# Optimization experiments

Hardware: AMD Instinct MI355X
Metric: run time of the kernel (lower is better)

## Reference

```python
import jax, jax.numpy as jnp
import numpy as np
from jax import lax

B, T, V, E, H, O = 32, 64, 30000, 64, 64, 7


def setup_inputs() -> dict:
    key = jax.random.key(0)
    ks = jax.random.split(key, 17)
    s_in = 1.0 / np.sqrt(E)
    s_h = 1.0 / np.sqrt(H)
    inp = {
        "x": jax.random.uniform(ks[0], (B, T, V), dtype=jnp.float32),
        "vocab_embed": 0.02 * jax.random.normal(ks[1], (V, E), dtype=jnp.float32),
        "W_ir": s_in * jax.random.normal(ks[2], (H, E), dtype=jnp.float32),
        "W_iz": s_in * jax.random.normal(ks[3], (H, E), dtype=jnp.float32),
        "W_in": s_in * jax.random.normal(ks[4], (H, E), dtype=jnp.float32),
        "W_hr": s_h * jax.random.normal(ks[5], (H, H), dtype=jnp.float32),
        "W_hz": s_h * jax.random.normal(ks[6], (H, H), dtype=jnp.float32),
        "W_hn": s_h * jax.random.normal(ks[7], (H, H), dtype=jnp.float32),
        "b_ir": s_h * jax.random.normal(ks[8], (H,), dtype=jnp.float32),
        "b_iz": s_h * jax.random.normal(ks[9], (H,), dtype=jnp.float32),
        "b_in": s_h * jax.random.normal(ks[10], (H,), dtype=jnp.float32),
        "b_hr": s_h * jax.random.normal(ks[11], (H,), dtype=jnp.float32),
        "b_hz": s_h * jax.random.normal(ks[12], (H,), dtype=jnp.float32),
        "b_hn": s_h * jax.random.normal(ks[13], (H,), dtype=jnp.float32),
        "W_out": s_h * jax.random.normal(ks[14], (O, H), dtype=jnp.float32),
        "b_out": s_h * jax.random.normal(ks[15], (O,), dtype=jnp.float32),
        "prediction_point": T,
    }
    return inp


def reference(x, vocab_embed, W_ir, W_iz, W_in, W_hr, W_hz, W_hn,
              b_ir, b_iz, b_in, b_hr, b_hz, b_hn, W_out, b_out,
              prediction_point):
    # embed_x = relu((x @ vocab_embed) / x.sum(-1, keepdims))  -> [B, T, E]
    embed_x = jax.nn.relu(jnp.einsum("btv,ve->bte", x, vocab_embed)
                          / jnp.sum(x, axis=2, keepdims=True))

    # t = 0: no hidden contribution at all (faithful to original)
    e0 = embed_x[:, 0, :]
    z1 = jax.nn.sigmoid(e0 @ W_iz.T + b_iz)
    n1 = jnp.tanh(e0 @ W_in.T + b_in)
    h0 = (1.0 - z1) * n1  # [B, H]

    def step(h, e_t):
        hr = h @ W_hr.T + b_hr
        r = jax.nn.sigmoid(e_t @ W_ir.T + b_ir + hr)
        z = jax.nn.sigmoid(e_t @ W_iz.T + b_iz + h @ W_hz.T + b_hz)
        # NOTE: original code uses hidden_reset (W_hr) here, not hidden_new
        n = jnp.tanh(e_t @ W_in.T + b_in + r * hr)
        h_new = (1.0 - z) * n + z * h
        return h_new, None

    # scan over t = 1 .. prediction_point-1
    es = jnp.swapaxes(embed_x[:, 1:prediction_point, :], 0, 1)  # [T-1, B, E]
    h_final, _ = lax.scan(step, h0, es)

    return h_final @ W_out.T + b_out  # [B, O] logits (prob=False)
```

## Files before the change

kernel.cpp:

```cpp
#include <hip/hip_runtime.h>
#include <hip/hip_bf16.h>

typedef unsigned short u16;
typedef short short8 __attribute__((ext_vector_type(8)));
typedef float floatx4 __attribute__((ext_vector_type(4)));

#define BB 32
#define TT 64
#define VV 30000
#define EE 64
#define HH 64
#define OO 7
#define KSPLIT 32
#define NU32 937
#define KTAIL0 29984

__device__ __forceinline__ u16 f2b(float f) {
    unsigned u = __float_as_uint(f);
    u += 0x7FFFu + ((u >> 16) & 1u);
    return (u16)(u >> 16);
}

__device__ __forceinline__ unsigned pk2(float fo, float fe) {
    return __builtin_amdgcn_perm(__float_as_uint(fo), __float_as_uint(fe), 0x07060302u);
}

__device__ __forceinline__ float sigmoid_f(float x) {
    return 1.f / (1.f + __expf(-x));
}

__device__ __forceinline__ float tanh_f(float x) {
    float a = fabsf(x);
    float e = __expf(-2.f * a);
    float t = (1.f - e) / (1.f + e);
    return x < 0.f ? -t : t;
}

__global__ __launch_bounds__(256) void kT(const float* __restrict__ VE, u16* __restrict__ VT) {
    __shared__ u16 tile[64][72];
    int v0 = blockIdx.x * 64;
    int t = threadIdx.x;
    #pragma unroll
    for (int i = 0; i < 4; ++i) {
        int c = i * 256 + t;
        int row = c >> 4, col4 = (c & 15) * 4;
        if (v0 + row < VV) {
            float4 d = *(const float4*)(VE + (size_t)(v0 + row) * EE + col4);
            ushort4 s;
            s.x = f2b(d.x); s.y = f2b(d.y); s.z = f2b(d.z); s.w = f2b(d.w);
            *(ushort4*)&tile[row][col4] = s;
        }
    }
    __syncthreads();
    int e0 = (t >> 6) * 16;
    int v = t & 63;
    if (v0 + v < VV) {
        #pragma unroll
        for (int ee = 0; ee < 16; ++ee) {
            int e = e0 + ee;
            VT[(size_t)e * VV + v0 + v] = tile[v][e];
        }
    }
}

__global__ __launch_bounds__(256) void kE(const float* __restrict__ x, const u16* __restrict__ vt,
                                          float* __restrict__ Cpart, float* __restrict__ Rpart) {
    int tid = threadIdx.x;
    int w = tid >> 6, l = tid & 63;
    int r15 = l & 15, q = l >> 4;
    int mb = blockIdx.x, kb = blockIdx.y;
    int m0 = mb * 64;
    int wr = m0 + w * 16;

    const float* aRow = x + (size_t)(wr + r15) * VV;
    const u16* b0p = vt + (size_t)(r15)      * VV;
    const u16* b1p = vt + (size_t)(16 + r15) * VV;
    const u16* b2p = vt + (size_t)(32 + r15) * VV;
    const u16* b3p = vt + (size_t)(48 + r15) * VV;

    floatx4 acc[4] = {};
    floatx4 accS = {};
    short8 ones;
    #pragma unroll
    for (int i = 0; i < 8; ++i) ones[i] = (short)0x3F80;

    int u0 = (kb * NU32) / KSPLIT, u1 = ((kb + 1) * NU32) / KSPLIT;

    #pragma unroll 2
    for (int u = u0; u < u1; ++u) {
        int k0 = u * 32 + q * 8;
        float4 a0 = *(const float4*)(aRow + k0);
        float4 a1 = *(const float4*)(aRow + k0 + 4);
        short8 bf0 = *(const short8*)(b0p + k0);
        short8 bf1 = *(const short8*)(b1p + k0);
        short8 bf2 = *(const short8*)(b2p + k0);
        short8 bf3 = *(const short8*)(b3p + k0);
        short8 af;
        unsigned* afu = (unsigned*)&af;
        afu[0] = pk2(a0.y, a0.x);
        afu[1] = pk2(a0.w, a0.z);
        afu[2] = pk2(a1.y, a1.x);
        afu[3] = pk2(a1.w, a1.z);
        acc[0] = __builtin_amdgcn_mfma_f32_16x16x32_bf16(af, bf0, acc[0], 0, 0, 0);
        acc[1] = __builtin_amdgcn_mfma_f32_16x16x32_bf16(af, bf1, acc[1], 0, 0, 0);
        acc[2] = __builtin_amdgcn_mfma_f32_16x16x32_bf16(af, bf2, acc[2], 0, 0, 0);
        acc[3] = __builtin_amdgcn_mfma_f32_16x16x32_bf16(af, bf3, acc[3], 0, 0, 0);
        accS   = __builtin_amdgcn_mfma_f32_16x16x32_bf16(af, ones, accS, 0, 0, 0);
    }

    if (kb == KSPLIT - 1) {
        short8 af, bf0, bf1, bf2, bf3;
        #pragma unroll
        for (int i = 0; i < 8; ++i) { af[i] = 0; bf0[i] = 0; bf1[i] = 0; bf2[i] = 0; bf3[i] = 0; }
        if (q < 2) {
            int k0 = KTAIL0 + q * 8;
            float4 a0 = *(const float4*)(aRow + k0);
            float4 a1 = *(const float4*)(aRow + k0 + 4);
            unsigned* afu = (unsigned*)&af;
            afu[0] = pk2(a0.y, a0.x);
            afu[1] = pk2(a0.w, a0.z);
            afu[2] = pk2(a1.y, a1.x);
            afu[3] = pk2(a1.w, a1.z);
            bf0 = *(const short8*)(b0p + k0);
            bf1 = *(const short8*)(b1p + k0);
            bf2 = *(const short8*)(b2p + k0);
            bf3 = *(const short8*)(b3p + k0);
        }
        acc[0] = __builtin_amdgcn_mfma_f32_16x16x32_bf16(af, bf0, acc[0], 0, 0, 0);
        acc[1] = __builtin_amdgcn_mfma_f32_16x16x32_bf16(af, bf1, acc[1], 0, 0, 0);
        acc[2] = __builtin_amdgcn_mfma_f32_16x16x32_bf16(af, bf2, acc[2], 0, 0, 0);
        acc[3] = __builtin_amdgcn_mfma_f32_16x16x32_bf16(af, bf3, acc[3], 0, 0, 0);
        accS   = __builtin_amdgcn_mfma_f32_16x16x32_bf16(af, ones, accS, 0, 0, 0);
    }

    float* Cp = Cpart + (size_t)kb * (2048 * 64);
    #pragma unroll
    for (int r = 0; r < 4; ++r) {
        int row = wr + q * 4 + r;
        #pragma unroll
        for (int n = 0; n < 4; ++n)
            Cp[(size_t)row * 64 + n * 16 + r15] = acc[n][r];
        if (r15 == 0) Rpart[kb * 2048 + row] = accS[r];
    }
}

__global__ __launch_bounds__(256) void kG2(const float* __restrict__ Cpart, const float* __restrict__ Rpart,
                                           const float* __restrict__ Wir, const float* __restrict__ Wiz,
                                           const float* __restrict__ Win,
                                           const float* __restrict__ bir, const float* __restrict__ biz,
                                           const float* __restrict__ bin,
                                           float* __restrict__ Xr, float* __restrict__ Xz,
                                           float* __restrict__ Xn, float* __restrict__ H0) {
    __shared__ __align__(16) u16 eL[64 * 72];
    __shared__ float rsinv[64];
    int tid = threadIdx.x;
    int m0 = blockIdx.x * 64;

    if (tid < 64) {
        float rs = 0.f;
        #pragma unroll
        for (int kb = 0; kb < KSPLIT; ++kb)
            rs += Rpart[kb * 2048 + m0 + tid];
        rsinv[tid] = 1.f / rs;
    }
    float4 a4[4];
    #pragma unroll
    for (int r = 0; r < 4; ++r) { a4[r].x = 0.f; a4[r].y = 0.f; a4[r].z = 0.f; a4[r].w = 0.f; }
    const float* cp = Cpart + (size_t)m0 * 64 + tid * 4;
    #pragma unroll 4
    for (int kb = 0; kb < KSPLIT; ++kb) {
        #pragma unroll
        for (int r = 0; r < 4; ++r) {
            float4 v = *(const float4*)(cp + (size_t)kb * (2048 * 64) + r * 1024);
            a4[r].x += v.x; a4[r].y += v.y; a4[r].z += v.z; a4[r].w += v.w;
        }
    }
    __syncthreads();
    #pragma unroll
    for (int r = 0; r < 4; ++r) {
        int m = r * 16 + (tid >> 4);
        float ri = rsinv[m];
        float e0 = a4[r].x * ri, e1 = a4[r].y * ri, e2 = a4[r].z * ri, e3 = a4[r].w * ri;
        e0 = e0 > 0.f ? e0 : 0.f;  e1 = e1 > 0.f ? e1 : 0.f;
        e2 = e2 > 0.f ? e2 : 0.f;  e3 = e3 > 0.f ? e3 : 0.f;
        ushort4 s;
        s.x = f2b(e0); s.y = f2b(e1); s.z = f2b(e2); s.w = f2b(e3);
        *(ushort4*)&eL[m * 72 + (tid & 15) * 4] = s;
    }
    __syncthreads();

    int w = tid >> 6, l = tid & 63;
    int r15 = l & 15, q = l >> 4;
    short8 a0 = *(const short8*)&eL[(w * 16 + r15) * 72 + q * 8];
    short8 a1 = *(const short8*)&eL[(w * 16 + r15) * 72 + 32 + q * 8];

    floatx4 acc[3][4] = {};
    const float* Wg0 = Wir; const float* Wg1 = Wiz; const float* Wg2 = Win;
    #pragma unroll
    for (int g = 0; g < 3; ++g) {
        const float* W = (g == 0) ? Wg0 : (g == 1) ? Wg1 : Wg2;
        #pragma unroll
        for (int nb = 0; nb < 4; ++nb) {
            const float* wrow = W + (nb * 16 + r15) * 64 + q * 8;
            float4 w0 = *(const float4*)(wrow);
            float4 w1 = *(const float4*)(wrow + 4);
            float4 w2 = *(const float4*)(wrow + 32);
            float4 w3 = *(const float4*)(wrow + 36);
            short8 b0, b1;
            unsigned* b0u = (unsigned*)&b0; unsigned* b1u = (unsigned*)&b1;
            b0u[0] = pk2(w0.y, w0.x); b0u[1] = pk2(w0.w, w0.z);
            b0u[2] = pk2(w1.y, w1.x); b0u[3] = pk2(w1.w, w1.z);
            b1u[0] = pk2(w2.y, w2.x); b1u[1] = pk2(w2.w, w2.z);
            b1u[2] = pk2(w3.y, w3.x); b1u[3] = pk2(w3.w, w3.z);
            acc[g][nb] = __builtin_amdgcn_mfma_f32_16x16x32_bf16(a0, b0, acc[g][nb], 0, 0, 0);
            acc[g][nb] = __builtin_amdgcn_mfma_f32_16x16x32_bf16(a1, b1, acc[g][nb], 0, 0, 0);
        }
    }

    #pragma unroll
    for (int g = 0; g < 3; ++g) {
        float* Xo = (g == 0) ? Xr : (g == 1) ? Xz : Xn;
        const float* bo = (g == 0) ? bir : (g == 1) ? biz : bin;
        #pragma unroll
        for (int nb = 0; nb < 4; ++nb) {
            int j = nb * 16 + r15;
            float bias = bo[j];
            #pragma unroll
            for (int r = 0; r < 4; ++r) {
                int m = m0 + w * 16 + q * 4 + r;
                Xo[(size_t)m * 64 + j] = acc[g][nb][r] + bias;
            }
        }
    }
    if (w == 0 && q == 0) {
        #pragma unroll
        for (int nb = 0; nb < 4; ++nb) {
            int j = nb * 16 + r15;
            float z1 = sigmoid_f(acc[1][nb][0] + biz[j]);
            float n1 = tanh_f(acc[2][nb][0] + bin[j]);
            H0[blockIdx.x * 64 + j] = (1.f - z1) * n1;
        }
    }
}

__global__ __launch_bounds__(256) void kS(const float* __restrict__ Xr, const float* __restrict__ Xz,
                                          const float* __restrict__ Xn, const float* __restrict__ H0,
                                          const float* __restrict__ Whr, const float* __restrict__ Whz,
                                          const float* __restrict__ bhr, const float* __restrict__ bhz,
                                          const float* __restrict__ Wout, const float* __restrict__ bout,
                                          float* __restrict__ out) {
    int b = blockIdx.x;
    int tid = threadIdx.x;
    int i = tid & 63, jw = tid >> 6;
    __shared__ float XsR[64 * 64], XsZ[64 * 64], XsN[64 * 64];
    __shared__ float h[64];
    __shared__ float P[4][2][64];

    const float* xr = Xr + (size_t)b * 4096;
    const float* xz = Xz + (size_t)b * 4096;
    const float* xn = Xn + (size_t)b * 4096;
    #pragma unroll
    for (int it = 0; it < 4; ++it) {
        int off = it * 1024 + tid * 4;
        *(float4*)&XsR[off] = *(const float4*)&xr[off];
        *(float4*)&XsZ[off] = *(const float4*)&xz[off];
        *(float4*)&XsN[off] = *(const float4*)&xn[off];
    }
    float wr[16], wz[16];
    #pragma unroll
    for (int jj = 0; jj < 16; ++jj) {
        wr[jj] = Whr[i * 64 + jw * 16 + jj];
        wz[jj] = Whz[i * 64 + jw * 16 + jj];
    }
    float bhr_i = bhr[i];
    float bhz_i = bhz[i];
    if (tid < 64) h[tid] = H0[b * 64 + tid];
    __syncthreads();

    for (int t = 1; t < 64; ++t) {
        float pr = 0.f, pz = 0.f;
        #pragma unroll
        for (int jj = 0; jj < 16; ++jj) {
            float hj = h[jw * 16 + jj];
            pr += hj * wr[jj];
            pz += hj * wz[jj];
        }
        P[jw][0][i] = pr;
        P[jw][1][i] = pz;
        __syncthreads();
        if (tid < 64) {
            float hr = bhr_i + P[0][0][i] + P[1][0][i] + P[2][0][i] + P[3][0][i];
            float hz = bhz_i + P[0][1][i] + P[1][1][i] + P[2][1][i] + P[3][1][i];
            float r = sigmoid_f(XsR[t * 64 + i] + hr);
            float z = sigmoid_f(XsZ[t * 64 + i] + hz);
            float n = tanh_f(XsN[t * 64 + i] + r * hr);
            h[i] = (1.f - z) * n + z * h[i];
        }
        __syncthreads();
    }

    if (tid < OO) {
        float acc2 = bout[tid];
        #pragma unroll 8
        for (int ii = 0; ii < 64; ++ii)
            acc2 += h[ii] * Wout[tid * 64 + ii];
        out[b * OO + tid] = acc2;
    }
}

extern "C" void kernel_launch(void* const* d_in, const int* in_sizes, int n_in,
                              void* d_out, int out_size, void* d_ws, size_t ws_size,
                              hipStream_t stream) {
    const float* x    = (const float*)d_in[0];
    const float* VE   = (const float*)d_in[1];
    const float* Wir  = (const float*)d_in[2];
    const float* Wiz  = (const float*)d_in[3];
    const float* Win  = (const float*)d_in[4];
    const float* Whr  = (const float*)d_in[5];
    const float* Whz  = (const float*)d_in[6];
    const float* bir  = (const float*)d_in[8];
    const float* biz  = (const float*)d_in[9];
    const float* bin  = (const float*)d_in[10];
    const float* bhr  = (const float*)d_in[11];
    const float* bhz  = (const float*)d_in[12];
    const float* Wout = (const float*)d_in[14];
    const float* bout = (const float*)d_in[15];

    char* ws = (char*)d_ws;
    u16*   VT    = (u16*)(ws);
    float* Cpart = (float*)(ws + 3840000);
    float* Rpart = (float*)(ws + 3840000 + 16777216);
    float* Xr    = (float*)(ws + 20879360);
    float* Xz    = (float*)(ws + 21403648);
    float* Xn    = (float*)(ws + 21927936);
    float* H0    = (float*)(ws + 22452224);

    kT<<<(VV + 63) / 64, 256, 0, stream>>>(VE, VT);
    kE<<<dim3(2048 / 64, KSPLIT), 256, 0, stream>>>(x, VT, Cpart, Rpart);
    kG2<<<32, 256, 0, stream>>>(Cpart, Rpart, Wir, Wiz, Win, bir, biz, bin, Xr, Xz, Xn, H0);
    kS<<<BB, 256, 0, stream>>>(Xr, Xz, Xn, H0, Whr, Whz, bhr, bhz, Wout, bout, (float*)d_out);
}
```

Measured before the change: 447.4 us.

## Pre-tile bf16 vocab embedding in MFMA fragment order; single-wave GRU scan with readlane

The transpose kernel now writes the bf16 embedding in a tiled fragment layout, with 32-k chunks laid out as [nb][r][k]. This lets each GEMM lane read its four B fragments from one contiguous 4 KB block instead of four rows strided by V, and it zero-pads the tail so the tail loads need no guard. The recurrent scan is rewritten to run on one 64-thread wave per batch row, with full W_hr/W_hz rows held in registers. The hidden state is broadcast with readlane, which removes shared-memory partial sums and the two barriers per timestep. The cost is higher register pressure (128 weight floats per thread) and a serial 64-term dot product per lane.

```diff
diff --git a/kernel.cpp b/kernel.cpp
--- a/kernel.cpp
+++ b/kernel.cpp
@@ -13,7 +13,6 @@
 #define OO 7
 #define KSPLIT 32
 #define NU32 937
-#define KTAIL0 29984
 
 __device__ __forceinline__ u16 f2b(float f) {
     unsigned u = __float_as_uint(f);
@@ -36,34 +35,37 @@
     return x < 0.f ? -t : t;
 }
 
-__global__ __launch_bounds__(256) void kT(const float* __restrict__ VE, u16* __restrict__ VT) {
+__global__ __launch_bounds__(256) void kT(const float* __restrict__ VE, u16* __restrict__ VTf) {
     __shared__ u16 tile[64][72];
     int v0 = blockIdx.x * 64;
     int t = threadIdx.x;
     #pragma unroll
-    for (int i = 0; i < 4; ++i) {
-        int c = i * 256 + t;
+    for (int it = 0; it < 4; ++it) {
+        int c = it * 256 + t;
         int row = c >> 4, col4 = (c & 15) * 4;
+        ushort4 s; s.x = 0; s.y = 0; s.z = 0; s.w = 0;
         if (v0 + row < VV) {
             float4 d = *(const float4*)(VE + (size_t)(v0 + row) * EE + col4);
-            ushort4 s;
             s.x = f2b(d.x); s.y = f2b(d.y); s.z = f2b(d.z); s.w = f2b(d.w);
-            *(ushort4*)&tile[row][col4] = s;
-        }
+        }
+        *(ushort4*)&tile[row][col4] = s;
     }
     __syncthreads();
-    int e0 = (t >> 6) * 16;
-    int v = t & 63;
-    if (v0 + v < VV) {
-        #pragma unroll
-        for (int ee = 0; ee < 16; ++ee) {
-            int e = e0 + ee;
-            VT[(size_t)e * VV + v0 + v] = tile[v][e];
-        }
-    }
-}
-
-__global__ __launch_bounds__(256) void kE(const float* __restrict__ x, const u16* __restrict__ vt,
+    int e = t & 63;
+    int nb = e >> 4, r = e & 15;
+    #pragma unroll
+    for (int half = 0; half < 2; ++half) {
+        int q8 = (t >> 6) + half * 4;
+        int u = (v0 >> 5) + (q8 >> 2);
+        int kin = (q8 & 3) * 8;
+        u16 tmp[8];
+        #pragma unroll
+        for (int jj = 0; jj < 8; ++jj) tmp[jj] = tile[q8 * 8 + jj][e];
+        *(uint4*)&VTf[(size_t)u * 2048 + nb * 512 + r * 32 + kin] = *(uint4*)tmp;
+    }
+}
+
+__global__ __launch_bounds__(256) void kE(const float* __restrict__ x, const u16* __restrict__ vtf,
                                           float* __restrict__ Cpart, float* __restrict__ Rpart) {
     int tid = threadIdx.x;
     int w = tid >> 6, l = tid & 63;
@@ -71,12 +73,10 @@
     int mb = blockIdx.x, kb = blockIdx.y;
     int m0 = mb * 64;
     int wr = m0 + w * 16;
-
-    const float* aRow = x + (size_t)(wr + r15) * VV;
-    const u16* b0p = vt + (size_t)(r15)      * VV;
-    const u16* b1p = vt + (size_t)(16 + r15) * VV;
-    const u16* b2p = vt + (size_t)(32 + r15) * VV;
-    const u16* b3p = vt + (size_t)(48 + r15) * VV;
+    int u0 = (kb * NU32) / KSPLIT, u1 = ((kb + 1) * NU32) / KSPLIT;
+
+    const float* aP = x + (size_t)(wr + r15) * VV + u0 * 32 + q * 8;
+    const u16*   bP = vtf + (size_t)u0 * 2048 + r15 * 32 + q * 8;
 
     floatx4 acc[4] = {};
     floatx4 accS = {};
@@ -84,17 +84,14 @@
     #pragma unroll
     for (int i = 0; i < 8; ++i) ones[i] = (short)0x3F80;
 
-    int u0 = (kb * NU32) / KSPLIT, u1 = ((kb + 1) * NU32) / KSPLIT;
-
     #pragma unroll 2
     for (int u = u0; u < u1; ++u) {
-        int k0 = u * 32 + q * 8;
-        float4 a0 = *(const float4*)(aRow + k0);
-        float4 a1 = *(const float4*)(aRow + k0 + 4);
-        short8 bf0 = *(const short8*)(b0p + k0);
-        short8 bf1 = *(const short8*)(b1p + k0);
-        short8 bf2 = *(const short8*)(b2p + k0);
-        short8 bf3 = *(const short8*)(b3p + k0);
+        float4 a0 = *(const float4*)(aP);
+        float4 a1 = *(const float4*)(aP + 4);
+        short8 bf0 = *(const short8*)(bP);
+        short8 bf1 = *(const short8*)(bP + 512);
+        short8 bf2 = *(const short8*)(bP + 1024);
+        short8 bf3 = *(const short8*)(bP + 1536);
         short8 af;
         unsigned* afu = (unsigned*)&af;
         afu[0] = pk2(a0.y, a0.x);
@@ -106,26 +103,27 @@
         acc[2] = __builtin_amdgcn_mfma_f32_16x16x32_bf16(af, bf2, acc[2], 0, 0, 0);
         acc[3] = __builtin_amdgcn_mfma_f32_16x16x32_bf16(af, bf3, acc[3], 0, 0, 0);
         accS   = __builtin_amdgcn_mfma_f32_16x16x32_bf16(af, ones, accS, 0, 0, 0);
+        aP += 32;
+        bP += 2048;
     }
 
     if (kb == KSPLIT - 1) {
-        short8 af, bf0, bf1, bf2, bf3;
-        #pragma unroll
-        for (int i = 0; i < 8; ++i) { af[i] = 0; bf0[i] = 0; bf1[i] = 0; bf2[i] = 0; bf3[i] = 0; }
+        short8 af;
+        #pragma unroll
+        for (int i = 0; i < 8; ++i) af[i] = 0;
         if (q < 2) {
-            int k0 = KTAIL0 + q * 8;
-            float4 a0 = *(const float4*)(aRow + k0);
-            float4 a1 = *(const float4*)(aRow + k0 + 4);
+            float4 a0 = *(const float4*)(aP);
+            float4 a1 = *(const float4*)(aP + 4);
             unsigned* afu = (unsigned*)&af;
             afu[0] = pk2(a0.y, a0.x);
             afu[1] = pk2(a0.w, a0.z);
             afu[2] = pk2(a1.y, a1.x);
             afu[3] = pk2(a1.w, a1.z);
-            bf0 = *(const short8*)(b0p + k0);
-            bf1 = *(const short8*)(b1p + k0);
-            bf2 = *(const short8*)(b2p + k0);
-            bf3 = *(const short8*)(b3p + k0);
-        }
+        }
+        short8 bf0 = *(const short8*)(bP);
+        short8 bf1 = *(const short8*)(bP + 512);
+        short8 bf2 = *(const short8*)(bP + 1024);
+        short8 bf3 = *(const short8*)(bP + 1536);
         acc[0] = __builtin_amdgcn_mfma_f32_16x16x32_bf16(af, bf0, acc[0], 0, 0, 0);
         acc[1] = __builtin_amdgcn_mfma_f32_16x16x32_bf16(af, bf1, acc[1], 0, 0, 0);
         acc[2] = __builtin_amdgcn_mfma_f32_16x16x32_bf16(af, bf2, acc[2], 0, 0, 0);
@@ -195,10 +193,9 @@
     short8 a1 = *(const short8*)&eL[(w * 16 + r15) * 72 + 32 + q * 8];
 
     floatx4 acc[3][4] = {};
-    const float* Wg0 = Wir; const float* Wg1 = Wiz; const float* Wg2 = Win;
     #pragma unroll
     for (int g = 0; g < 3; ++g) {
-        const float* W = (g == 0) ? Wg0 : (g == 1) ? Wg1 : Wg2;
+        const float* W = (g == 0) ? Wir : (g == 1) ? Wiz : Win;
         #pragma unroll
         for (int nb = 0; nb < 4; ++nb) {
             const float* wrow = W + (nb * 16 + r15) * 64 + q * 8;
@@ -243,68 +240,70 @@
     }
 }
 
-__global__ __launch_bounds__(256) void kS(const float* __restrict__ Xr, const float* __restrict__ Xz,
+__global__ __launch_bounds__(64) void kS2(const float* __restrict__ Xr, const float* __restrict__ Xz,
                                           const float* __restrict__ Xn, const float* __restrict__ H0,
                                           const float* __restrict__ Whr, const float* __restrict__ Whz,
                                           const float* __restrict__ bhr, const float* __restrict__ bhz,
                                           const float* __restrict__ Wout, const float* __restrict__ bout,
                                           float* __restrict__ out) {
     int b = blockIdx.x;
-    int tid = threadIdx.x;
-    int i = tid & 63, jw = tid >> 6;
-    __shared__ float XsR[64 * 64], XsZ[64 * 64], XsN[64 * 64];
-    __shared__ float h[64];
-    __shared__ float P[4][2][64];
-
-    const float* xr = Xr + (size_t)b * 4096;
-    const float* xz = Xz + (size_t)b * 4096;
-    const float* xn = Xn + (size_t)b * 4096;
-    #pragma unroll
-    for (int it = 0; it < 4; ++it) {
-        int off = it * 1024 + tid * 4;
-        *(float4*)&XsR[off] = *(const float4*)&xr[off];
-        *(float4*)&XsZ[off] = *(const float4*)&xz[off];
-        *(float4*)&XsN[off] = *(const float4*)&xn[off];
-    }
-    float wr[16], wz[16];
-    #pragma unroll
-    for (int jj = 0; jj < 16; ++jj) {
-        wr[jj] = Whr[i * 64 + jw * 16 + jj];
-        wz[jj] = Whz[i * 64 + jw * 16 + jj];
-    }
-    float bhr_i = bhr[i];
-    float bhz_i = bhz[i];
-    if (tid < 64) h[tid] = H0[b * 64 + tid];
+    int i = threadIdx.x;
+    __shared__ float Xs[3][64][64];
+    __shared__ float hsh[64];
+
+    const float* s0 = Xr + (size_t)b * 4096;
+    const float* s1 = Xz + (size_t)b * 4096;
+    const float* s2 = Xn + (size_t)b * 4096;
+    #pragma unroll
+    for (int c = 0; c < 16; ++c) {
+        int off = (c * 64 + i) * 4;
+        *(float4*)&Xs[0][0][off] = *(const float4*)(s0 + off);
+        *(float4*)&Xs[1][0][off] = *(const float4*)(s1 + off);
+        *(float4*)&Xs[2][0][off] = *(const float4*)(s2 + off);
+    }
+    float wrg[64], wzg[64];
+    #pragma unroll
+    for (int c = 0; c < 16; ++c) {
+        float4 v1 = *(const float4*)(Whr + i * 64 + c * 4);
+        float4 v2 = *(const float4*)(Whz + i * 64 + c * 4);
+        wrg[c * 4 + 0] = v1.x; wrg[c * 4 + 1] = v1.y; wrg[c * 4 + 2] = v1.z; wrg[c * 4 + 3] = v1.w;
+        wzg[c * 4 + 0] = v2.x; wzg[c * 4 + 1] = v2.y; wzg[c * 4 + 2] = v2.z; wzg[c * 4 + 3] = v2.w;
+    }
+    float h = H0[b * 64 + i];
+    float bri = bhr[i], bzi = bhz[i];
+
+    for (int t = 1; t < 64; ++t) {
+        float xr = Xs[0][t][i], xz = Xs[1][t][i], xn = Xs[2][t][i];
+        float p0 = 0.f, p1 = 0.f, p2 = 0.f, p3 = 0.f;
+        float z0 = 0.f, z1 = 0.f, z2 = 0.f, z3 = 0.f;
+        unsigned hu = __float_as_uint(h);
+        #pragma unroll
+        for (int j = 0; j < 64; j += 4) {
+            float h0 = __uint_as_float(__builtin_amdgcn_readlane(hu, j + 0));
+            float h1 = __uint_as_float(__builtin_amdgcn_readlane(hu, j + 1));
+            float h2 = __uint_as_float(__builtin_amdgcn_readlane(hu, j + 2));
+            float h3 = __uint_as_float(__builtin_amdgcn_readlane(hu, j + 3));
+            p0 += h0 * wrg[j + 0]; p1 += h1 * wrg[j + 1];
+            p2 += h2 * wrg[j + 2]; p3 += h3 * wrg[j + 3];
+            z0 += h0 * wzg[j + 0]; z1 += h1 * wzg[j + 1];
+            z2 += h2 * wzg[j + 2]; z3 += h3 * wzg[j + 3];
+        }
+        float hr = bri + ((p0 + p1) + (p2 + p3));
+        float hz = bzi + ((z0 + z1) + (z2 + z3));
+        float r = sigmoid_f(xr + hr);
+        float z = sigmoid_f(xz + hz);
+        float n = tanh_f(xn + r * hr);
+        h = (1.f - z) * n + z * h;
+    }
+
+    hsh[i] = h;
     __syncthreads();
-
-    for (int t = 1; t < 64; ++t) {
-        float pr = 0.f, pz = 0.f;
-        #pragma unroll
-        for (int jj = 0; jj < 16; ++jj) {
-            float hj = h[jw * 16 + jj];
-            pr += hj * wr[jj];
-            pz += hj * wz[jj];
-        }
-        P[jw][0][i] = pr;
-        P[jw][1][i] = pz;
-        __syncthreads();
-        if (tid < 64) {
-            float hr = bhr_i + P[0][0][i] + P[1][0][i] + P[2][0][i] + P[3][0][i];
-            float hz = bhz_i + P[0][1][i] + P[1][1][i] + P[2][1][i] + P[3][1][i];
-            float r = sigmoid_f(XsR[t * 64 + i] + hr);
-            float z = sigmoid_f(XsZ[t * 64 + i] + hz);
-            float n = tanh_f(XsN[t * 64 + i] + r * hr);
-            h[i] = (1.f - z) * n + z * h[i];
-        }
-        __syncthreads();
-    }
-
-    if (tid < OO) {
-        float acc2 = bout[tid];
+    if (i < OO) {
+        float a = bout[i];
         #pragma unroll 8
-        for (int ii = 0; ii < 64; ++ii)
-            acc2 += h[ii] * Wout[tid * 64 + ii];
-        out[b * OO + tid] = acc2;
+        for (int j = 0; j < 64; ++j)
+            a += hsh[j] * Wout[i * 64 + j];
+        out[b * OO + i] = a;
     }
 }
 
@@ -327,16 +326,16 @@
     const float* bout = (const float*)d_in[15];
 
     char* ws = (char*)d_ws;
-    u16*   VT    = (u16*)(ws);
-    float* Cpart = (float*)(ws + 3840000);
-    float* Rpart = (float*)(ws + 3840000 + 16777216);
-    float* Xr    = (float*)(ws + 20879360);
-    float* Xz    = (float*)(ws + 21403648);
-    float* Xn    = (float*)(ws + 21927936);
-    float* H0    = (float*)(ws + 22452224);
-
-    kT<<<(VV + 63) / 64, 256, 0, stream>>>(VE, VT);
-    kE<<<dim3(2048 / 64, KSPLIT), 256, 0, stream>>>(x, VT, Cpart, Rpart);
+    u16*   VTf   = (u16*)(ws);
+    float* Cpart = (float*)(ws + 4000000);
+    float* Rpart = (float*)(ws + 20777216);
+    float* Xr    = (float*)(ws + 21039360);
+    float* Xz    = (float*)(ws + 21563648);
+    float* Xn    = (float*)(ws + 22087936);
+    float* H0    = (float*)(ws + 22612224);
+
+    kT<<<469, 256, 0, stream>>>(VE, VTf);
+    kE<<<dim3(2048 / 64, KSPLIT), 256, 0, stream>>>(x, VTf, Cpart, Rpart);
     kG2<<<32, 256, 0, stream>>>(Cpart, Rpart, Wir, Wiz, Win, bir, biz, bin, Xr, Xz, Xn, H0);
-    kS<<<BB, 256, 0, stream>>>(Xr, Xz, Xn, H0, Whr, Whz, bhr, bhz, Wout, bout, (float*)d_out);
-}
+    kS2<<<BB, 64, 0, stream>>>(Xr, Xz, Xn, H0, Whr, Whz, bhr, bhz, Wout, bout, (float*)d_out);
+}
```

Measured after the change: 435.3 us. -2.7%, faster.
